# Performance work log

Measured on AMD Instinct MI355X. Metric: run time of the kernel, lower is better.

The kernel has to match this reference:

```python
import jax, jax.numpy as jnp
import numpy as np
import itertools

DIM_X, DIM_Y = 3, 3
MAX_DIGIT = DIM_X * DIM_Y          # 9
NUM_NODES = MAX_DIGIT ** 2         # 81
EMBED = 16
HID = 96
BATCH = 256
ITERS = 4


def determine_edges(dim_x, dim_y):
    md = dim_x * dim_y
    rows = []
    for r in range(md):
        for c in range(md):
            s = {(r, i) for i in range(md)} | {(i, c) for i in range(md)}
            xm, ym = r // dim_x * dim_x, c // dim_y * dim_y
            s |= set(itertools.product(range(xm, xm + dim_x), range(ym, ym + dim_y)))
            s -= {(r, c)}
            rows.append(sorted(i * md + j for i, j in s))
    return np.asarray(rows, dtype=np.int32)  # [81, 20]


def mlp3(x, w0, b0, w1, b1, w2, b2):
    # MLP([a,b,c,d]): two ReLU hidden layers, linear output
    x = jax.nn.relu(x @ w0.T + b0)
    x = jax.nn.relu(x @ w1.T + b1)
    return x @ w2.T + b2


def setup_inputs() -> dict:
    key = jax.random.key(0)
    keys = iter(jax.random.split(key, 40))

    def lin(din, dout):
        kw, kb = jax.random.split(next(keys))
        lim = 1.0 / np.sqrt(din)
        w = jax.random.uniform(kw, (dout, din), jnp.float32, -lim, lim)
        b = jax.random.uniform(kb, (dout,), jnp.float32, -lim, lim)
        return w, b

    embed = jax.random.normal(next(keys), (MAX_DIGIT + 1, EMBED), jnp.float32)

    in_w0, in_b0 = lin(EMBED, HID); in_w1, in_b1 = lin(HID, HID); in_w2, in_b2 = lin(HID, HID)
    f_w0, f_b0 = lin(2 * HID, HID); f_w1, f_b1 = lin(HID, HID); f_w2, f_b2 = lin(HID, HID)
    g_w0, g_b0 = lin(2 * HID, HID); g_w1, g_b1 = lin(HID, HID); g_w2, g_b2 = lin(HID, HID)
    r_w0, r_b0 = lin(HID, HID); r_w1, r_b1 = lin(HID, HID); r_w2, r_b2 = lin(HID, MAX_DIGIT)

    lim = 1.0 / np.sqrt(HID)
    lstm_wih = jax.random.uniform(next(keys), (4 * HID, HID), jnp.float32, -lim, lim)
    lstm_whh = jax.random.uniform(next(keys), (4 * HID, HID), jnp.float32, -lim, lim)
    lstm_bih = jax.random.uniform(next(keys), (4 * HID,), jnp.float32, -lim, lim)
    lstm_bhh = jax.random.uniform(next(keys), (4 * HID,), jnp.float32, -lim, lim)

    grids = jax.random.randint(next(keys), (BATCH, NUM_NODES), 0, MAX_DIGIT + 1)
    c0 = jax.random.normal(next(keys), (BATCH * NUM_NODES, HID), jnp.float32)
    edges = jnp.asarray(determine_edges(DIM_X, DIM_Y))

    return dict(embed=embed,
                in_w0=in_w0, in_b0=in_b0, in_w1=in_w1, in_b1=in_b1, in_w2=in_w2, in_b2=in_b2,
                f_w0=f_w0, f_b0=f_b0, f_w1=f_w1, f_b1=f_b1, f_w2=f_w2, f_b2=f_b2,
                g_w0=g_w0, g_b0=g_b0, g_w1=g_w1, g_b1=g_b1, g_w2=g_w2, g_b2=g_b2,
                lstm_wih=lstm_wih, lstm_whh=lstm_whh, lstm_bih=lstm_bih, lstm_bhh=lstm_bhh,
                r_w0=r_w0, r_b0=r_b0, r_w1=r_w1, r_b1=r_b1, r_w2=r_w2, r_b2=r_b2,
                c0=c0, grids=grids, edges=edges, iters=ITERS)


def reference(embed,
              in_w0, in_b0, in_w1, in_b1, in_w2, in_b2,
              f_w0, f_b0, f_w1, f_b1, f_w2, f_b2,
              g_w0, g_b0, g_w1, g_b1, g_w2, g_b2,
              lstm_wih, lstm_whh, lstm_bih, lstm_bhh,
              r_w0, r_b0, r_w1, r_b1, r_w2, r_b2,
              c0, grids, edges, iters):
    B, N = grids.shape
    K = edges.shape[1]
    emb = embed[grids]                                   # [B, N, EMBED]
    X = mlp3(emb, in_w0, in_b0, in_w1, in_b1, in_w2, in_b2)  # [B, N, HID]
    H = X
    h = X.reshape(B * N, HID)
    c = c0
    outputs = []
    for _ in range(iters):
        # gather neighbor states: [B, N, K, HID]
        Hn = H[:, edges]
        Hs = jnp.broadcast_to(H[:, :, None, :], Hn.shape)
        pair = jnp.concatenate([Hs, Hn], axis=-1)        # [B, N, K, 2*HID]
        M = mlp3(pair, f_w0, f_b0, f_w1, f_b1, f_w2, f_b2).sum(axis=2)  # [B, N, HID]
        gin = mlp3(jnp.concatenate([X, M], axis=-1),
                   g_w0, g_b0, g_w1, g_b1, g_w2, g_b2).reshape(B * N, HID)
        # single-step LSTM (torch gate order: i, f, g, o)
        gates = gin @ lstm_wih.T + lstm_bih + h @ lstm_whh.T + lstm_bhh
        gi, gf, gg, go = jnp.split(gates, 4, axis=-1)
        c = jax.nn.sigmoid(gf) * c + jax.nn.sigmoid(gi) * jnp.tanh(gg)
        h = jax.nn.sigmoid(go) * jnp.tanh(c)
        H = h.reshape(B, N, HID)
        outputs.append(mlp3(H, r_w0, r_b0, r_w1, r_b1, r_w2, r_b2))  # [B, N, MAX_DIGIT]
    return jnp.stack(outputs)  # [iters, B, N, MAX_DIGIT]
```

## Files before the change

### kernel.cpp

```cpp
#include <hip/hip_runtime.h>
#include <hip/hip_bf16.h>

typedef __hip_bfloat16 bf16;
typedef __attribute__((ext_vector_type(8))) short short8;
typedef __attribute__((ext_vector_type(8))) __bf16 bf16x8;
typedef __attribute__((ext_vector_type(4))) float f32x4;

#define BN 20736
#define NNODE 81
#define KNB 20

__device__ inline float bf2f(short s) {
  union { unsigned u; float f; } x; x.u = ((unsigned)(unsigned short)s) << 16; return x.f;
}
__device__ inline short f2bf(float f) {
  __hip_bfloat16 h = __float2bfloat16(f);
  return *reinterpret_cast<short*>(&h);
}

__device__ inline void load_w96(const bf16* __restrict__ W, int ldw, int lr, int lq,
                                bf16x8 wf[6][3]) {
  #pragma unroll
  for (int nt = 0; nt < 6; ++nt)
    #pragma unroll
    for (int ks = 0; ks < 3; ++ks)
      wf[nt][ks] = __builtin_bit_cast(bf16x8,
          *(const short8*)&W[(size_t)(nt * 16 + lr) * ldw + ks * 32 + lq * 8]);
}
__device__ inline void zacc6(f32x4 acc[6]) {
  #pragma unroll
  for (int nt = 0; nt < 6; ++nt) acc[nt] = (f32x4){0.f, 0.f, 0.f, 0.f};
}
__device__ inline void gemm96(const bf16x8 af[3], const bf16x8 wf[6][3], f32x4 acc[6]) {
  #pragma unroll
  for (int ks = 0; ks < 3; ++ks)
    #pragma unroll
    for (int nt = 0; nt < 6; ++nt)
      acc[nt] = __builtin_amdgcn_mfma_f32_16x16x32_bf16(af[ks], wf[nt][ks], acc[nt], 0, 0, 0);
}
__device__ inline void acc_to_xbuf(float* xw, const f32x4 acc[6], int lr, int lq) {
  #pragma unroll
  for (int nt = 0; nt < 6; ++nt)
    #pragma unroll
    for (int r = 0; r < 4; ++r)
      xw[(lq * 4 + r) * 100 + nt * 16 + lr] = acc[nt][r];
}
__device__ inline void xbuf_frag(const float* xw, int lr, int lq,
                                 const float* __restrict__ bias, float bscale,
                                 const bf16* __restrict__ residRow, int act,
                                 bf16x8 af[3]) {
  #pragma unroll
  for (int ks = 0; ks < 3; ++ks) {
    const int c0 = ks * 32 + lq * 8;
    float4 x0 = *(const float4*)&xw[lr * 100 + c0];
    float4 x1 = *(const float4*)&xw[lr * 100 + c0 + 4];
    float xv[8] = {x0.x, x0.y, x0.z, x0.w, x1.x, x1.y, x1.z, x1.w};
    if (bias) {
      float4 b0 = *(const float4*)&bias[c0];
      float4 b1 = *(const float4*)&bias[c0 + 4];
      float bv[8] = {b0.x, b0.y, b0.z, b0.w, b1.x, b1.y, b1.z, b1.w};
      #pragma unroll
      for (int j = 0; j < 8; ++j) xv[j] += bscale * bv[j];
    }
    if (residRow) {
      short8 r8 = *(const short8*)&residRow[c0];
      #pragma unroll
      for (int j = 0; j < 8; ++j) xv[j] += bf2f(r8[j]);
    }
    short8 o;
    #pragma unroll
    for (int j = 0; j < 8; ++j) {
      float v = xv[j];
      if (act) v = fmaxf(v, 0.f);
      o[j] = f2bf(v);
    }
    af[ks] = __builtin_bit_cast(bf16x8, o);
  }
}
__device__ inline void store_frag(bf16* dst, int lq, const bf16x8 af[3]) {
  #pragma unroll
  for (int ks = 0; ks < 3; ++ks)
    *(short8*)&dst[ks * 32 + lq * 8] = __builtin_bit_cast(short8, af[ks]);
}

__global__ __launch_bounds__(256) void prep_k(
    const float* in_w1, const float* in_w2, const float* f_w1, const float* f_w2,
    const float* g_w1, const float* g_w2, const float* r_w0, const float* r_w1,
    const float* r_w2, const float* wih, const float* whh, const float* g_w0,
    const float* f_w0, const float* in_w0, const float* f_b0,
    bf16* inw1b, bf16* inw2b, bf16* fw1b, bf16* fw2b,
    bf16* gw1b, bf16* gw2b, bf16* rw0b, bf16* rw1b,
    bf16* rw2b, bf16* wihb, bf16* whhb, bf16* gw0b,
    bf16* wfnb, bf16* w0pb, float* bias_fn)
{
  int idx = blockIdx.x * 256 + threadIdx.x;
  int y = blockIdx.y;
  const float* src = nullptr; bf16* dst = nullptr; int cnt = 0;
  switch (y) {
    case 0:  src = in_w1; dst = inw1b; cnt = 9216;  break;
    case 1:  src = in_w2; dst = inw2b; cnt = 9216;  break;
    case 2:  src = f_w1;  dst = fw1b;  cnt = 9216;  break;
    case 3:  src = f_w2;  dst = fw2b;  cnt = 9216;  break;
    case 4:  src = g_w1;  dst = gw1b;  cnt = 9216;  break;
    case 5:  src = g_w2;  dst = gw2b;  cnt = 9216;  break;
    case 6:  src = r_w0;  dst = rw0b;  cnt = 9216;  break;
    case 7:  src = r_w1;  dst = rw1b;  cnt = 9216;  break;
    case 8:  src = r_w2;  dst = rw2b;  cnt = 864;   break;
    case 9:  src = wih;   dst = wihb;  cnt = 36864; break;
    case 10: src = whh;   dst = whhb;  cnt = 36864; break;
    case 11: src = g_w0;  dst = gw0b;  cnt = 18432; break;
    case 12: {
      if (idx < 18432) {
        int n = idx / 96, k = idx - n * 96;
        float v = (n < 96) ? f_w0[n * 192 + k] : f_w0[(n - 96) * 192 + 96 + k];
        wfnb[idx] = __float2bfloat16(v);
      }
      return;
    }
    case 13: {
      if (idx < 3072) {
        int n = idx >> 5, k = idx & 31;
        w0pb[idx] = __float2bfloat16(k < 16 ? in_w0[n * 16 + k] : 0.f);
      }
      return;
    }
    default: {
      if (idx < 192) bias_fn[idx] = (idx < 96) ? f_b0[idx] : 0.f;
      return;
    }
  }
  if (idx < cnt) dst[idx] = __float2bfloat16(src[idx]);
}

__global__ __launch_bounds__(256) void embed_k(const float* __restrict__ embed,
                                               const int* __restrict__ grids,
                                               bf16* __restrict__ emb) {
  int idx = blockIdx.x * 256 + threadIdx.x;
  if (idx >= BN * 32) return;
  int r = idx >> 5, k = idx & 31;
  emb[idx] = __float2bfloat16(k < 16 ? embed[grids[r] * 16 + k] : 0.f);
}

__global__ __launch_bounds__(256) void fused_in_k(
    const bf16* __restrict__ emb, const bf16* __restrict__ w0pb, const float* __restrict__ in_b0,
    const bf16* __restrict__ inw1b, const float* __restrict__ in_b1,
    const bf16* __restrict__ inw2b, const float* __restrict__ in_b2,
    const bf16* __restrict__ gw0b, const float* __restrict__ g_b0,
    const bf16* __restrict__ wfnb, const float* __restrict__ bias_fn,
    bf16* __restrict__ X, bf16* __restrict__ Xg, bf16* __restrict__ P)
{
  __shared__ float xbuf[4 * 1600];
  const int t = threadIdx.x, w = t >> 6, lane = t & 63, lr = lane & 15, lq = lane >> 4;
  const int m0 = blockIdx.x * 64 + w * 16;
  float* xw = xbuf + w * 1600;
  bf16x8 wf[6][3]; f32x4 acc[6]; bf16x8 af[3];

  bf16x8 a0 = __builtin_bit_cast(bf16x8, *(const short8*)&emb[(size_t)(m0 + lr) * 32 + lq * 8]);
  #pragma unroll
  for (int nt = 0; nt < 6; ++nt)
    wf[nt][0] = __builtin_bit_cast(bf16x8, *(const short8*)&w0pb[(size_t)(nt * 16 + lr) * 32 + lq * 8]);
  zacc6(acc);
  #pragma unroll
  for (int nt = 0; nt < 6; ++nt)
    acc[nt] = __builtin_amdgcn_mfma_f32_16x16x32_bf16(a0, wf[nt][0], acc[nt], 0, 0, 0);
  acc_to_xbuf(xw, acc, lr, lq); xbuf_frag(xw, lr, lq, in_b0, 1.f, nullptr, 1, af);
  load_w96(inw1b, 96, lr, lq, wf); zacc6(acc); gemm96(af, wf, acc);
  acc_to_xbuf(xw, acc, lr, lq); xbuf_frag(xw, lr, lq, in_b1, 1.f, nullptr, 1, af);
  load_w96(inw2b, 96, lr, lq, wf); zacc6(acc); gemm96(af, wf, acc);
  acc_to_xbuf(xw, acc, lr, lq);
  bf16x8 xf[3];
  xbuf_frag(xw, lr, lq, in_b2, 1.f, nullptr, 0, xf);
  store_frag(&X[(size_t)(m0 + lr) * 96], lq, xf);
  load_w96(gw0b, 192, lr, lq, wf); zacc6(acc); gemm96(xf, wf, acc);
  acc_to_xbuf(xw, acc, lr, lq); xbuf_frag(xw, lr, lq, g_b0, 1.f, nullptr, 0, af);
  store_frag(&Xg[(size_t)(m0 + lr) * 96], lq, af);
  #pragma unroll
  for (int ph = 0; ph < 2; ++ph) {
    load_w96(wfnb + (size_t)ph * 96 * 96, 96, lr, lq, wf); zacc6(acc); gemm96(xf, wf, acc);
    acc_to_xbuf(xw, acc, lr, lq); xbuf_frag(xw, lr, lq, bias_fn + ph * 96, 1.f, nullptr, 0, af);
    store_frag(&P[(size_t)(m0 + lr) * 192 + ph * 96], lq, af);
  }
}

__global__ __launch_bounds__(256) void edge_k(
    const bf16* __restrict__ P, const bf16* __restrict__ w1bf,
    const float* __restrict__ b1, const int* __restrict__ edges,
    bf16* __restrict__ S)
{
  __shared__ short zs[160 * 104];
  const int t = threadIdx.x;
  const int ng0 = blockIdx.x * 2;
  for (int cc = t; cc < 160 * 12; cc += 256) {
    int zrow = cc / 12, c8 = cc - zrow * 12;
    int g = zrow >= 80 ? 1 : 0;
    int row = zrow - g * 80;
    int p = row / 20, j = row - p * 20;
    int gr = (ng0 + g) * 4 + p;
    int b = gr / NNODE, i = gr - b * NNODE;
    int e = edges[i * KNB + j];
    short8 a8 = *(const short8*)&P[(size_t)gr * 192 + c8 * 8];
    short8 n8 = *(const short8*)&P[((size_t)b * NNODE + e) * 192 + 96 + c8 * 8];
    short8 z;
    #pragma unroll
    for (int q = 0; q < 8; ++q)
      z[q] = f2bf(fmaxf(bf2f(a8[q]) + bf2f(n8[q]), 0.f));
    *(short8*)&zs[zrow * 104 + c8 * 8] = z;
  }
  __syncthreads();

  const int w = t >> 6, lane = t & 63, lr = lane & 15, lq = lane >> 4;
  const int g = w >> 1, ch = w & 1, n0 = ch * 48, zb = g * 80;
  const int row0 = (ng0 + g) * 4;

  bf16x8 wf[3][3];
  #pragma unroll
  for (int nt = 0; nt < 3; ++nt)
    #pragma unroll
    for (int ks = 0; ks < 3; ++ks)
      wf[nt][ks] = __builtin_bit_cast(bf16x8,
          *(const short8*)&w1bf[(size_t)(n0 + nt * 16 + lr) * 96 + ks * 32 + lq * 8]);

  f32x4 acc[5][3];
  #pragma unroll
  for (int mt = 0; mt < 5; ++mt)
    #pragma unroll
    for (int nt = 0; nt < 3; ++nt) acc[mt][nt] = (f32x4){0.f, 0.f, 0.f, 0.f};

  #pragma unroll
  for (int ks = 0; ks < 3; ++ks) {
    const int koff = ks * 32 + lq * 8;
    #pragma unroll
    for (int mt = 0; mt < 5; ++mt) {
      bf16x8 af = __builtin_bit_cast(bf16x8, *(const short8*)&zs[(zb + mt * 16 + lr) * 104 + koff]);
      #pragma unroll
      for (int nt = 0; nt < 3; ++nt)
        acc[mt][nt] = __builtin_amdgcn_mfma_f32_16x16x32_bf16(af, wf[nt][ks], acc[mt][nt], 0, 0, 0);
    }
  }

  float bv[3];
  #pragma unroll
  for (int nt = 0; nt < 3; ++nt) bv[nt] = b1[n0 + nt * 16 + lr];
  float nodeacc[4][3];
  #pragma unroll
  for (int pp = 0; pp < 4; ++pp)
    #pragma unroll
    for (int nt = 0; nt < 3; ++nt) nodeacc[pp][nt] = 0.f;
  #pragma unroll
  for (int mt = 0; mt < 5; ++mt)
    #pragma unroll
    for (int nt = 0; nt < 3; ++nt)
      #pragma unroll
      for (int r = 0; r < 4; ++r) {
        int row = mt * 16 + lq * 4 + r;
        int p = row / 20;
        float v = fmaxf(acc[mt][nt][r] + bv[nt], 0.f);
        #pragma unroll
        for (int pp = 0; pp < 4; ++pp)
          nodeacc[pp][nt] += (p == pp) ? v : 0.f;
      }
  #pragma unroll
  for (int pp = 0; pp < 4; ++pp)
    #pragma unroll
    for (int nt = 0; nt < 3; ++nt) {
      float v = nodeacc[pp][nt];
      v += __shfl_xor(v, 16, 64);
      v += __shfl_xor(v, 32, 64);
      if (lq == 0)
        S[(size_t)(row0 + pp) * 96 + n0 + nt * 16 + lr] = __float2bfloat16(v);
    }
}

__global__ __launch_bounds__(256) void fused_mlp_k(
    const bf16* __restrict__ S, const bf16* __restrict__ fw2b, const float* __restrict__ f_b2,
    const bf16* __restrict__ gw0b, const bf16* __restrict__ Xg,
    const bf16* __restrict__ gw1b, const float* __restrict__ g_b1,
    const bf16* __restrict__ gw2b, const float* __restrict__ g_b2,
    bf16* __restrict__ gin)
{
  __shared__ float xbuf[4 * 1600];
  const int t = threadIdx.x, w = t >> 6, lane = t & 63, lr = lane & 15, lq = lane >> 4;
  const int m0 = blockIdx.x * 64 + w * 16;
  float* xw = xbuf + w * 1600;
  bf16x8 wf[6][3]; f32x4 acc[6]; bf16x8 af[3];

  #pragma unroll
  for (int ks = 0; ks < 3; ++ks)
    af[ks] = __builtin_bit_cast(bf16x8, *(const short8*)&S[(size_t)(m0 + lr) * 96 + ks * 32 + lq * 8]);
  load_w96(fw2b, 96, lr, lq, wf); zacc6(acc); gemm96(af, wf, acc);
  acc_to_xbuf(xw, acc, lr, lq); xbuf_frag(xw, lr, lq, f_b2, (float)KNB, nullptr, 0, af);
  load_w96(gw0b + 96, 192, lr, lq, wf); zacc6(acc); gemm96(af, wf, acc);
  acc_to_xbuf(xw, acc, lr, lq);
  xbuf_frag(xw, lr, lq, nullptr, 0.f, &Xg[(size_t)(m0 + lr) * 96], 1, af);
  load_w96(gw1b, 96, lr, lq, wf); zacc6(acc); gemm96(af, wf, acc);
  acc_to_xbuf(xw, acc, lr, lq); xbuf_frag(xw, lr, lq, g_b1, 1.f, nullptr, 1, af);
  load_w96(gw2b, 96, lr, lq, wf); zacc6(acc); gemm96(af, wf, acc);
  acc_to_xbuf(xw, acc, lr, lq); xbuf_frag(xw, lr, lq, g_b2, 1.f, nullptr, 0, af);
  store_frag(&gin[(size_t)(m0 + lr) * 96], lq, af);
}

__global__ __launch_bounds__(256) void lstm_k(
    const bf16* __restrict__ gin, const bf16* __restrict__ Hin,
    const bf16* __restrict__ wihb, const bf16* __restrict__ whhb,
    const float* __restrict__ bih, const float* __restrict__ bhh,
    float* __restrict__ c, bf16* __restrict__ Hout)
{
  const int gslot = blockIdx.x * 4 + (threadIdx.x >> 6);
  const int rt = gslot / 6, knt = gslot - rt * 6;
  const int lane = threadIdx.x & 63, lr = lane & 15, lq = lane >> 4;
  const int m0 = rt * 16, kcol = knt * 16 + lr;

  f32x4 acc[4];
  #pragma unroll
  for (int g = 0; g < 4; ++g) acc[g] = (f32x4){0.f, 0.f, 0.f, 0.f};
  #pragma unroll
  for (int ks = 0; ks < 3; ++ks) {
    const int koff = ks * 32 + lq * 8;
    bf16x8 gf_ = __builtin_bit_cast(bf16x8, *(const short8*)&gin[(size_t)(m0 + lr) * 96 + koff]);
    bf16x8 hf_ = __builtin_bit_cast(bf16x8, *(const short8*)&Hin[(size_t)(m0 + lr) * 96 + koff]);
    #pragma unroll
    for (int g = 0; g < 4; ++g) {
      bf16x8 wi = __builtin_bit_cast(bf16x8, *(const short8*)&wihb[(size_t)(g * 96 + kcol) * 96 + koff]);
      acc[g] = __builtin_amdgcn_mfma_f32_16x16x32_bf16(gf_, wi, acc[g], 0, 0, 0);
      bf16x8 wh = __builtin_bit_cast(bf16x8, *(const short8*)&whhb[(size_t)(g * 96 + kcol) * 96 + koff]);
      acc[g] = __builtin_amdgcn_mfma_f32_16x16x32_bf16(hf_, wh, acc[g], 0, 0, 0);
    }
  }
  float bv[4];
  #pragma unroll
  for (int g = 0; g < 4; ++g) bv[g] = bih[g * 96 + kcol] + bhh[g * 96 + kcol];
  #pragma unroll
  for (int r = 0; r < 4; ++r) {
    int m = m0 + lq * 4 + r;
    size_t idx = (size_t)m * 96 + kcol;
    float gi = acc[0][r] + bv[0];
    float gf = acc[1][r] + bv[1];
    float gg = acc[2][r] + bv[2];
    float go = acc[3][r] + bv[3];
    float si = 1.f / (1.f + expf(-gi));
    float sf = 1.f / (1.f + expf(-gf));
    float so = 1.f / (1.f + expf(-go));
    float tg = tanhf(gg);
    float cn = sf * c[idx] + si * tg;
    c[idx] = cn;
    Hout[idx] = __float2bfloat16(so * tanhf(cn));
  }
}

__global__ __launch_bounds__(256) void fused_out_k(
    const bf16* __restrict__ H,
    const bf16* __restrict__ wfnb, const float* __restrict__ bias_fn, bf16* __restrict__ P,
    const bf16* __restrict__ rw0b, const float* __restrict__ r_b0,
    const bf16* __restrict__ rw1b, const float* __restrict__ r_b1,
    const bf16* __restrict__ rw2b, const float* __restrict__ r_b2,
    float* __restrict__ outp)
{
  __shared__ float xbuf[4 * 1600];
  const int t = threadIdx.x, w = t >> 6, lane = t & 63, lr = lane & 15, lq = lane >> 4;
  const int m0 = blockIdx.x * 64 + w * 16;
  float* xw = xbuf + w * 1600;
  bf16x8 wf[6][3]; f32x4 acc[6]; bf16x8 af[3];

  bf16x8 hf[3];
  #pragma unroll
  for (int ks = 0; ks < 3; ++ks)
    hf[ks] = __builtin_bit_cast(bf16x8, *(const short8*)&H[(size_t)(m0 + lr) * 96 + ks * 32 + lq * 8]);

  #pragma unroll
  for (int ph = 0; ph < 2; ++ph) {
    load_w96(wfnb + (size_t)ph * 96 * 96, 96, lr, lq, wf); zacc6(acc); gemm96(hf, wf, acc);
    acc_to_xbuf(xw, acc, lr, lq); xbuf_frag(xw, lr, lq, bias_fn + ph * 96, 1.f, nullptr, 0, af);
    store_frag(&P[(size_t)(m0 + lr) * 192 + ph * 96], lq, af);
  }
  load_w96(rw0b, 96, lr, lq, wf); zacc6(acc); gemm96(hf, wf, acc);
  acc_to_xbuf(xw, acc, lr, lq); xbuf_frag(xw, lr, lq, r_b0, 1.f, nullptr, 1, af);
  load_w96(rw1b, 96, lr, lq, wf); zacc6(acc); gemm96(af, wf, acc);
  acc_to_xbuf(xw, acc, lr, lq); xbuf_frag(xw, lr, lq, r_b1, 1.f, nullptr, 1, af);
  bf16x8 w9[3];
  #pragma unroll
  for (int ks = 0; ks < 3; ++ks) {
    short8 s = {0, 0, 0, 0, 0, 0, 0, 0};
    if (lr < 9) s = *(const short8*)&rw2b[(size_t)lr * 96 + ks * 32 + lq * 8];
    w9[ks] = __builtin_bit_cast(bf16x8, s);
  }
  f32x4 a9 = (f32x4){0.f, 0.f, 0.f, 0.f};
  #pragma unroll
  for (int ks = 0; ks < 3; ++ks)
    a9 = __builtin_amdgcn_mfma_f32_16x16x32_bf16(af[ks], w9[ks], a9, 0, 0, 0);
  if (lr < 9) {
    float bb = r_b2[lr];
    #pragma unroll
    for (int r = 0; r < 4; ++r)
      outp[(size_t)(m0 + lq * 4 + r) * 9 + lr] = a9[r] + bb;
  }
}

extern "C" void kernel_launch(void* const* d_in, const int* in_sizes, int n_in,
                              void* d_out, int out_size, void* d_ws, size_t ws_size,
                              hipStream_t stream) {
  const float* embed   = (const float*)d_in[0];
  const float* in_w0   = (const float*)d_in[1];
  const float* in_b0   = (const float*)d_in[2];
  const float* in_w1   = (const float*)d_in[3];
  const float* in_b1   = (const float*)d_in[4];
  const float* in_w2   = (const float*)d_in[5];
  const float* in_b2   = (const float*)d_in[6];
  const float* f_w0    = (const float*)d_in[7];
  const float* f_b0    = (const float*)d_in[8];
  const float* f_w1    = (const float*)d_in[9];
  const float* f_b1    = (const float*)d_in[10];
  const float* f_w2    = (const float*)d_in[11];
  const float* f_b2    = (const float*)d_in[12];
  const float* g_w0    = (const float*)d_in[13];
  const float* g_b0    = (const float*)d_in[14];
  const float* g_w1    = (const float*)d_in[15];
  const float* g_b1    = (const float*)d_in[16];
  const float* g_w2    = (const float*)d_in[17];
  const float* g_b2    = (const float*)d_in[18];
  const float* wih     = (const float*)d_in[19];
  const float* whh     = (const float*)d_in[20];
  const float* bih     = (const float*)d_in[21];
  const float* bhh     = (const float*)d_in[22];
  const float* r_w0    = (const float*)d_in[23];
  const float* r_b0    = (const float*)d_in[24];
  const float* r_w1    = (const float*)d_in[25];
  const float* r_b1    = (const float*)d_in[26];
  const float* r_w2    = (const float*)d_in[27];
  const float* r_b2    = (const float*)d_in[28];
  const float* c0      = (const float*)d_in[29];
  const int*   grids   = (const int*)d_in[30];
  const int*   edges   = (const int*)d_in[31];

  float* out = (float*)d_out;
  const int iters = out_size / (BN * 9);

  float* c    = (float*)d_ws;
  bf16* H0    = (bf16*)(c + (size_t)BN * 96);
  bf16* H1    = H0 + (size_t)BN * 96;
  bf16* Xg    = H1 + (size_t)BN * 96;
  bf16* P     = Xg + (size_t)BN * 96;
  bf16* S     = P  + (size_t)BN * 192;
  bf16* gin   = S  + (size_t)BN * 96;
  bf16* emb   = gin + (size_t)BN * 96;
  bf16* w0pb  = emb + (size_t)BN * 32;
  bf16* wfnb  = w0pb + 3072;
  bf16* inw1b = wfnb + 18432;
  bf16* inw2b = inw1b + 9216;
  bf16* fw1b  = inw2b + 9216;
  bf16* fw2b  = fw1b + 9216;
  bf16* gw0b  = fw2b + 9216;
  bf16* gw1b  = gw0b + 18432;
  bf16* gw2b  = gw1b + 9216;
  bf16* rw0b  = gw2b + 9216;
  bf16* rw1b  = rw0b + 9216;
  bf16* rw2b  = rw1b + 9216;
  bf16* wihb  = rw2b + 864;
  bf16* whhb  = wihb + 36864;
  float* bias_fn = (float*)(whhb + 36864);

  prep_k<<<dim3(144, 15), 256, 0, stream>>>(
      in_w1, in_w2, f_w1, f_w2, g_w1, g_w2, r_w0, r_w1, r_w2, wih, whh, g_w0,
      f_w0, in_w0, f_b0,
      inw1b, inw2b, fw1b, fw2b, gw1b, gw2b, rw0b, rw1b, rw2b, wihb, whhb, gw0b,
      wfnb, w0pb, bias_fn);
  embed_k<<<(BN * 32) / 256, 256, 0, stream>>>(embed, grids, emb);
  fused_in_k<<<BN / 64, 256, 0, stream>>>(emb, w0pb, in_b0, inw1b, in_b1, inw2b, in_b2,
                                          gw0b, g_b0, wfnb, bias_fn, H0, Xg, P);
  hipMemcpyAsync(c, c0, (size_t)BN * 96 * sizeof(float), hipMemcpyDeviceToDevice, stream);

  for (int it = 0; it < iters; ++it) {
    bf16* Hin  = (it & 1) ? H1 : H0;
    bf16* Hout = (it & 1) ? H0 : H1;
    edge_k<<<BN / 8, 256, 0, stream>>>(P, fw1b, f_b1, edges, S);
    fused_mlp_k<<<BN / 64, 256, 0, stream>>>(S, fw2b, f_b2, gw0b, Xg, gw1b, g_b1,
                                             gw2b, g_b2, gin);
    lstm_k<<<BN * 6 / 64, 256, 0, stream>>>(gin, Hin, wihb, whhb, bih, bhh, c, Hout);
    fused_out_k<<<BN / 64, 256, 0, stream>>>(Hout, wfnb, bias_fn, P, rw0b, r_b0,
                                             rw1b, r_b1, rw2b, r_b2,
                                             out + (size_t)it * BN * 9);
  }
}
```

Baseline: 370.7 us.

## Split MLP chain N-dimension across wave pairs and fuse f_w2 into edge kernel

The fused MLP kernels now have two waves share each 16-row tile, each computing 48 of the 96 output columns, with block-level barriers to exchange activations through shared memory. Each block therefore covers 32 rows instead of 64, which doubles the grid and halves the weight registers held per wave. Separately, the second edge-MLP GEMM (f_w2 applied to the summed messages, plus the bias times KNB) moves into edge_k via a small padded shared-memory tile. This removes one GEMM and the S round trip from fused_mlp_k, at the cost of extra __syncthreads, duplicated A-operand work across wave pairs, and only two waves active in the edge tail.

```diff
diff --git a/kernel.cpp b/kernel.cpp
--- a/kernel.cpp
+++ b/kernel.cpp
@@ -18,32 +18,32 @@
   return *reinterpret_cast<short*>(&h);
 }
 
-__device__ inline void load_w96(const bf16* __restrict__ W, int ldw, int lr, int lq,
-                                bf16x8 wf[6][3]) {
-  #pragma unroll
-  for (int nt = 0; nt < 6; ++nt)
+__device__ inline void zacc3(f32x4 acc[3]) {
+  #pragma unroll
+  for (int nt = 0; nt < 3; ++nt) acc[nt] = (f32x4){0.f, 0.f, 0.f, 0.f};
+}
+__device__ inline void load_w48(const bf16* __restrict__ W, int ldw, int n0, int lr, int lq,
+                                bf16x8 wf[3][3]) {
+  #pragma unroll
+  for (int nt = 0; nt < 3; ++nt)
     #pragma unroll
     for (int ks = 0; ks < 3; ++ks)
       wf[nt][ks] = __builtin_bit_cast(bf16x8,
-          *(const short8*)&W[(size_t)(nt * 16 + lr) * ldw + ks * 32 + lq * 8]);
-}
-__device__ inline void zacc6(f32x4 acc[6]) {
-  #pragma unroll
-  for (int nt = 0; nt < 6; ++nt) acc[nt] = (f32x4){0.f, 0.f, 0.f, 0.f};
-}
-__device__ inline void gemm96(const bf16x8 af[3], const bf16x8 wf[6][3], f32x4 acc[6]) {
+          *(const short8*)&W[(size_t)(n0 + nt * 16 + lr) * ldw + ks * 32 + lq * 8]);
+}
+__device__ inline void gemm48(const bf16x8 af[3], const bf16x8 wf[3][3], f32x4 acc[3]) {
   #pragma unroll
   for (int ks = 0; ks < 3; ++ks)
     #pragma unroll
-    for (int nt = 0; nt < 6; ++nt)
+    for (int nt = 0; nt < 3; ++nt)
       acc[nt] = __builtin_amdgcn_mfma_f32_16x16x32_bf16(af[ks], wf[nt][ks], acc[nt], 0, 0, 0);
 }
-__device__ inline void acc_to_xbuf(float* xw, const f32x4 acc[6], int lr, int lq) {
-  #pragma unroll
-  for (int nt = 0; nt < 6; ++nt)
+__device__ inline void acc_store_cs(float* xw, const f32x4 acc[3], int lr, int lq, int n0) {
+  #pragma unroll
+  for (int nt = 0; nt < 3; ++nt)
     #pragma unroll
     for (int r = 0; r < 4; ++r)
-      xw[(lq * 4 + r) * 100 + nt * 16 + lr] = acc[nt][r];
+      xw[(lq * 4 + r) * 100 + n0 + nt * 16 + lr] = acc[nt][r];
 }
 __device__ inline void xbuf_frag(const float* xw, int lr, int lq,
                                  const float* __restrict__ bias, float bscale,
@@ -149,47 +149,63 @@
     const bf16* __restrict__ wfnb, const float* __restrict__ bias_fn,
     bf16* __restrict__ X, bf16* __restrict__ Xg, bf16* __restrict__ P)
 {
-  __shared__ float xbuf[4 * 1600];
+  __shared__ float xbuf[2][2][1600];
   const int t = threadIdx.x, w = t >> 6, lane = t & 63, lr = lane & 15, lq = lane >> 4;
-  const int m0 = blockIdx.x * 64 + w * 16;
-  float* xw = xbuf + w * 1600;
-  bf16x8 wf[6][3]; f32x4 acc[6]; bf16x8 af[3];
+  const int mh = w >> 1, ch = w & 1, n0 = ch * 48;
+  const int m0 = blockIdx.x * 32 + mh * 16;
+  float* x0 = xbuf[0][mh];
+  float* x1 = xbuf[1][mh];
+  bf16x8 wf[3][3]; f32x4 acc[3]; bf16x8 af[3];
 
   bf16x8 a0 = __builtin_bit_cast(bf16x8, *(const short8*)&emb[(size_t)(m0 + lr) * 32 + lq * 8]);
   #pragma unroll
-  for (int nt = 0; nt < 6; ++nt)
-    wf[nt][0] = __builtin_bit_cast(bf16x8, *(const short8*)&w0pb[(size_t)(nt * 16 + lr) * 32 + lq * 8]);
-  zacc6(acc);
-  #pragma unroll
-  for (int nt = 0; nt < 6; ++nt)
+  for (int nt = 0; nt < 3; ++nt)
+    wf[nt][0] = __builtin_bit_cast(bf16x8,
+        *(const short8*)&w0pb[(size_t)(n0 + nt * 16 + lr) * 32 + lq * 8]);
+  zacc3(acc);
+  #pragma unroll
+  for (int nt = 0; nt < 3; ++nt)
     acc[nt] = __builtin_amdgcn_mfma_f32_16x16x32_bf16(a0, wf[nt][0], acc[nt], 0, 0, 0);
-  acc_to_xbuf(xw, acc, lr, lq); xbuf_frag(xw, lr, lq, in_b0, 1.f, nullptr, 1, af);
-  load_w96(inw1b, 96, lr, lq, wf); zacc6(acc); gemm96(af, wf, acc);
-  acc_to_xbuf(xw, acc, lr, lq); xbuf_frag(xw, lr, lq, in_b1, 1.f, nullptr, 1, af);
-  load_w96(inw2b, 96, lr, lq, wf); zacc6(acc); gemm96(af, wf, acc);
-  acc_to_xbuf(xw, acc, lr, lq);
+  acc_store_cs(x0, acc, lr, lq, n0);
+  __syncthreads();
+  xbuf_frag(x0, lr, lq, in_b0, 1.f, nullptr, 1, af);
+  load_w48(inw1b, 96, n0, lr, lq, wf); zacc3(acc); gemm48(af, wf, acc);
+  acc_store_cs(x1, acc, lr, lq, n0);
+  __syncthreads();
+  xbuf_frag(x1, lr, lq, in_b1, 1.f, nullptr, 1, af);
+  load_w48(inw2b, 96, n0, lr, lq, wf); zacc3(acc); gemm48(af, wf, acc);
+  acc_store_cs(x0, acc, lr, lq, n0);
+  __syncthreads();
   bf16x8 xf[3];
-  xbuf_frag(xw, lr, lq, in_b2, 1.f, nullptr, 0, xf);
-  store_frag(&X[(size_t)(m0 + lr) * 96], lq, xf);
-  load_w96(gw0b, 192, lr, lq, wf); zacc6(acc); gemm96(xf, wf, acc);
-  acc_to_xbuf(xw, acc, lr, lq); xbuf_frag(xw, lr, lq, g_b0, 1.f, nullptr, 0, af);
-  store_frag(&Xg[(size_t)(m0 + lr) * 96], lq, af);
+  xbuf_frag(x0, lr, lq, in_b2, 1.f, nullptr, 0, xf);
+  if (ch == 0) store_frag(&X[(size_t)(m0 + lr) * 96], lq, xf);
+  load_w48(gw0b, 192, n0, lr, lq, wf); zacc3(acc); gemm48(xf, wf, acc);
+  acc_store_cs(x1, acc, lr, lq, n0);
+  __syncthreads();
+  xbuf_frag(x1, lr, lq, g_b0, 1.f, nullptr, 0, af);
+  if (ch == 0) store_frag(&Xg[(size_t)(m0 + lr) * 96], lq, af);
   #pragma unroll
   for (int ph = 0; ph < 2; ++ph) {
-    load_w96(wfnb + (size_t)ph * 96 * 96, 96, lr, lq, wf); zacc6(acc); gemm96(xf, wf, acc);
-    acc_to_xbuf(xw, acc, lr, lq); xbuf_frag(xw, lr, lq, bias_fn + ph * 96, 1.f, nullptr, 0, af);
-    store_frag(&P[(size_t)(m0 + lr) * 192 + ph * 96], lq, af);
+    float* xb = ph ? x1 : x0;
+    load_w48(wfnb + (size_t)ph * 96 * 96, 96, n0, lr, lq, wf); zacc3(acc); gemm48(xf, wf, acc);
+    acc_store_cs(xb, acc, lr, lq, n0);
+    __syncthreads();
+    xbuf_frag(xb, lr, lq, bias_fn + ph * 96, 1.f, nullptr, 0, af);
+    if (ch == 0) store_frag(&P[(size_t)(m0 + lr) * 192 + ph * 96], lq, af);
   }
 }
 
 __global__ __launch_bounds__(256) void edge_k(
     const bf16* __restrict__ P, const bf16* __restrict__ w1bf,
     const float* __restrict__ b1, const int* __restrict__ edges,
-    bf16* __restrict__ S)
+    const bf16* __restrict__ fw2b, const float* __restrict__ f_b2,
+    bf16* __restrict__ M)
 {
   __shared__ short zs[160 * 104];
+  __shared__ short sbuf[16 * 104];
   const int t = threadIdx.x;
   const int ng0 = blockIdx.x * 2;
+  for (int i = t; i < 8 * 104; i += 256) sbuf[(8 + i / 104) * 104 + (i % 104)] = 0;
   for (int cc = t; cc < 160 * 12; cc += 256) {
     int zrow = cc / 12, c8 = cc - zrow * 12;
     int g = zrow >= 80 ? 1 : 0;
@@ -210,7 +226,6 @@
 
   const int w = t >> 6, lane = t & 63, lr = lane & 15, lq = lane >> 4;
   const int g = w >> 1, ch = w & 1, n0 = ch * 48, zb = g * 80;
-  const int row0 = (ng0 + g) * 4;
 
   bf16x8 wf[3][3];
   #pragma unroll
@@ -267,36 +282,73 @@
       v += __shfl_xor(v, 16, 64);
       v += __shfl_xor(v, 32, 64);
       if (lq == 0)
-        S[(size_t)(row0 + pp) * 96 + n0 + nt * 16 + lr] = __float2bfloat16(v);
-    }
+        sbuf[(g * 4 + pp) * 104 + n0 + nt * 16 + lr] = f2bf(v);
+    }
+  __syncthreads();
+  if (w < 2) {
+    const int mn0 = w * 48;
+    bf16x8 mwf[3][3];
+    #pragma unroll
+    for (int nt = 0; nt < 3; ++nt)
+      #pragma unroll
+      for (int ks = 0; ks < 3; ++ks)
+        mwf[nt][ks] = __builtin_bit_cast(bf16x8,
+            *(const short8*)&fw2b[(size_t)(mn0 + nt * 16 + lr) * 96 + ks * 32 + lq * 8]);
+    f32x4 macc[3];
+    zacc3(macc);
+    #pragma unroll
+    for (int ks = 0; ks < 3; ++ks) {
+      bf16x8 af = __builtin_bit_cast(bf16x8, *(const short8*)&sbuf[lr * 104 + ks * 32 + lq * 8]);
+      #pragma unroll
+      for (int nt = 0; nt < 3; ++nt)
+        macc[nt] = __builtin_amdgcn_mfma_f32_16x16x32_bf16(af, mwf[nt][ks], macc[nt], 0, 0, 0);
+    }
+    #pragma unroll
+    for (int nt = 0; nt < 3; ++nt) {
+      int col = mn0 + nt * 16 + lr;
+      float bb = (float)KNB * f_b2[col];
+      #pragma unroll
+      for (int r = 0; r < 4; ++r) {
+        int row = lq * 4 + r;
+        if (row < 8)
+          M[(size_t)(ng0 * 4 + row) * 96 + col] = __float2bfloat16(macc[nt][r] + bb);
+      }
+    }
+  }
 }
 
 __global__ __launch_bounds__(256) void fused_mlp_k(
-    const bf16* __restrict__ S, const bf16* __restrict__ fw2b, const float* __restrict__ f_b2,
+    const bf16* __restrict__ Min,
     const bf16* __restrict__ gw0b, const bf16* __restrict__ Xg,
     const bf16* __restrict__ gw1b, const float* __restrict__ g_b1,
     const bf16* __restrict__ gw2b, const float* __restrict__ g_b2,
     bf16* __restrict__ gin)
 {
-  __shared__ float xbuf[4 * 1600];
+  __shared__ float xbuf[2][2][1600];
   const int t = threadIdx.x, w = t >> 6, lane = t & 63, lr = lane & 15, lq = lane >> 4;
-  const int m0 = blockIdx.x * 64 + w * 16;
-  float* xw = xbuf + w * 1600;
-  bf16x8 wf[6][3]; f32x4 acc[6]; bf16x8 af[3];
+  const int mh = w >> 1, ch = w & 1, n0 = ch * 48;
+  const int m0 = blockIdx.x * 32 + mh * 16;
+  float* x0 = xbuf[0][mh];
+  float* x1 = xbuf[1][mh];
+  bf16x8 wf[3][3]; f32x4 acc[3]; bf16x8 af[3];
 
   #pragma unroll
   for (int ks = 0; ks < 3; ++ks)
-    af[ks] = __builtin_bit_cast(bf16x8, *(const short8*)&S[(size_t)(m0 + lr) * 96 + ks * 32 + lq * 8]);
-  load_w96(fw2b, 96, lr, lq, wf); zacc6(acc); gemm96(af, wf, acc);
-  acc_to_xbuf(xw, acc, lr, lq); xbuf_frag(xw, lr, lq, f_b2, (float)KNB, nullptr, 0, af);
-  load_w96(gw0b + 96, 192, lr, lq, wf); zacc6(acc); gemm96(af, wf, acc);
-  acc_to_xbuf(xw, acc, lr, lq);
-  xbuf_frag(xw, lr, lq, nullptr, 0.f, &Xg[(size_t)(m0 + lr) * 96], 1, af);
-  load_w96(gw1b, 96, lr, lq, wf); zacc6(acc); gemm96(af, wf, acc);
-  acc_to_xbuf(xw, acc, lr, lq); xbuf_frag(xw, lr, lq, g_b1, 1.f, nullptr, 1, af);
-  load_w96(gw2b, 96, lr, lq, wf); zacc6(acc); gemm96(af, wf, acc);
-  acc_to_xbuf(xw, acc, lr, lq); xbuf_frag(xw, lr, lq, g_b2, 1.f, nullptr, 0, af);
-  store_frag(&gin[(size_t)(m0 + lr) * 96], lq, af);
+    af[ks] = __builtin_bit_cast(bf16x8,
+        *(const short8*)&Min[(size_t)(m0 + lr) * 96 + ks * 32 + lq * 8]);
+  load_w48(gw0b + 96, 192, n0, lr, lq, wf); zacc3(acc); gemm48(af, wf, acc);
+  acc_store_cs(x0, acc, lr, lq, n0);
+  __syncthreads();
+  xbuf_frag(x0, lr, lq, nullptr, 0.f, &Xg[(size_t)(m0 + lr) * 96], 1, af);
+  load_w48(gw1b, 96, n0, lr, lq, wf); zacc3(acc); gemm48(af, wf, acc);
+  acc_store_cs(x1, acc, lr, lq, n0);
+  __syncthreads();
+  xbuf_frag(x1, lr, lq, g_b1, 1.f, nullptr, 1, af);
+  load_w48(gw2b, 96, n0, lr, lq, wf); zacc3(acc); gemm48(af, wf, acc);
+  acc_store_cs(x0, acc, lr, lq, n0);
+  __syncthreads();
+  xbuf_frag(x0, lr, lq, g_b2, 1.f, nullptr, 0, af);
+  if (ch == 0) store_frag(&gin[(size_t)(m0 + lr) * 96], lq, af);
 }
 
 __global__ __launch_bounds__(256) void lstm_k(
@@ -355,43 +407,55 @@
     const bf16* __restrict__ rw2b, const float* __restrict__ r_b2,
     float* __restrict__ outp)
 {
-  __shared__ float xbuf[4 * 1600];
+  __shared__ float xbuf[2][2][1600];
   const int t = threadIdx.x, w = t >> 6, lane = t & 63, lr = lane & 15, lq = lane >> 4;
-  const int m0 = blockIdx.x * 64 + w * 16;
-  float* xw = xbuf + w * 1600;
-  bf16x8 wf[6][3]; f32x4 acc[6]; bf16x8 af[3];
+  const int mh = w >> 1, ch = w & 1, n0 = ch * 48;
+  const int m0 = blockIdx.x * 32 + mh * 16;
+  float* x0 = xbuf[0][mh];
+  float* x1 = xbuf[1][mh];
+  bf16x8 wf[3][3]; f32x4 acc[3]; bf16x8 af[3];
 
   bf16x8 hf[3];
   #pragma unroll
   for (int ks = 0; ks < 3; ++ks)
-    hf[ks] = __builtin_bit_cast(bf16x8, *(const short8*)&H[(size_t)(m0 + lr) * 96 + ks * 32 + lq * 8]);
+    hf[ks] = __builtin_bit_cast(bf16x8,
+        *(const short8*)&H[(size_t)(m0 + lr) * 96 + ks * 32 + lq * 8]);
 
   #pragma unroll
   for (int ph = 0; ph < 2; ++ph) {
-    load_w96(wfnb + (size_t)ph * 96 * 96, 96, lr, lq, wf); zacc6(acc); gemm96(hf, wf, acc);
-    acc_to_xbuf(xw, acc, lr, lq); xbuf_frag(xw, lr, lq, bias_fn + ph * 96, 1.f, nullptr, 0, af);
-    store_frag(&P[(size_t)(m0 + lr) * 192 + ph * 96], lq, af);
-  }
-  load_w96(rw0b, 96, lr, lq, wf); zacc6(acc); gemm96(hf, wf, acc);
-  acc_to_xbuf(xw, acc, lr, lq); xbuf_frag(xw, lr, lq, r_b0, 1.f, nullptr, 1, af);
-  load_w96(rw1b, 96, lr, lq, wf); zacc6(acc); gemm96(af, wf, acc);
-  acc_to_xbuf(xw, acc, lr, lq); xbuf_frag(xw, lr, lq, r_b1, 1.f, nullptr, 1, af);
-  bf16x8 w9[3];
-  #pragma unroll
-  for (int ks = 0; ks < 3; ++ks) {
-    short8 s = {0, 0, 0, 0, 0, 0, 0, 0};
-    if (lr < 9) s = *(const short8*)&rw2b[(size_t)lr * 96 + ks * 32 + lq * 8];
-    w9[ks] = __builtin_bit_cast(bf16x8, s);
-  }
-  f32x4 a9 = (f32x4){0.f, 0.f, 0.f, 0.f};
-  #pragma unroll
-  for (int ks = 0; ks < 3; ++ks)
-    a9 = __builtin_amdgcn_mfma_f32_16x16x32_bf16(af[ks], w9[ks], a9, 0, 0, 0);
-  if (lr < 9) {
-    float bb = r_b2[lr];
-    #pragma unroll
-    for (int r = 0; r < 4; ++r)
-      outp[(size_t)(m0 + lq * 4 + r) * 9 + lr] = a9[r] + bb;
+    float* xb = ph ? x1 : x0;
+    load_w48(wfnb + (size_t)ph * 96 * 96, 96, n0, lr, lq, wf); zacc3(acc); gemm48(hf, wf, acc);
+    acc_store_cs(xb, acc, lr, lq, n0);
+    __syncthreads();
+    xbuf_frag(xb, lr, lq, bias_fn + ph * 96, 1.f, nullptr, 0, af);
+    if (ch == 0) store_frag(&P[(size_t)(m0 + lr) * 192 + ph * 96], lq, af);
+  }
+  load_w48(rw0b, 96, n0, lr, lq, wf); zacc3(acc); gemm48(hf, wf, acc);
+  acc_store_cs(x0, acc, lr, lq, n0);
+  __syncthreads();
+  xbuf_frag(x0, lr, lq, r_b0, 1.f, nullptr, 1, af);
+  load_w48(rw1b, 96, n0, lr, lq, wf); zacc3(acc); gemm48(af, wf, acc);
+  acc_store_cs(x1, acc, lr, lq, n0);
+  __syncthreads();
+  xbuf_frag(x1, lr, lq, r_b1, 1.f, nullptr, 1, af);
+  if (ch == 0) {
+    bf16x8 w9[3];
+    #pragma unroll
+    for (int ks = 0; ks < 3; ++ks) {
+      short8 s = {0, 0, 0, 0, 0, 0, 0, 0};
+      if (lr < 9) s = *(const short8*)&rw2b[(size_t)lr * 96 + ks * 32 + lq * 8];
+      w9[ks] = __builtin_bit_cast(bf16x8, s);
+    }
+    f32x4 a9 = (f32x4){0.f, 0.f, 0.f, 0.f};
+    #pragma unroll
+    for (int ks = 0; ks < 3; ++ks)
+      a9 = __builtin_amdgcn_mfma_f32_16x16x32_bf16(af[ks], w9[ks], a9, 0, 0, 0);
+    if (lr < 9) {
+      float bb = r_b2[lr];
+      #pragma unroll
+      for (int r = 0; r < 4; ++r)
+        outp[(size_t)(m0 + lq * 4 + r) * 9 + lr] = a9[r] + bb;
+    }
   }
 }
 
@@ -439,8 +503,8 @@
   bf16* H1    = H0 + (size_t)BN * 96;
   bf16* Xg    = H1 + (size_t)BN * 96;
   bf16* P     = Xg + (size_t)BN * 96;
-  bf16* S     = P  + (size_t)BN * 192;
-  bf16* gin   = S  + (size_t)BN * 96;
+  bf16* Mb    = P  + (size_t)BN * 192;
+  bf16* gin   = Mb + (size_t)BN * 96;
   bf16* emb   = gin + (size_t)BN * 96;
   bf16* w0pb  = emb + (size_t)BN * 32;
   bf16* wfnb  = w0pb + 3072;
@@ -464,18 +528,17 @@
       inw1b, inw2b, fw1b, fw2b, gw1b, gw2b, rw0b, rw1b, rw2b, wihb, whhb, gw0b,
       wfnb, w0pb, bias_fn);
   embed_k<<<(BN * 32) / 256, 256, 0, stream>>>(embed, grids, emb);
-  fused_in_k<<<BN / 64, 256, 0, stream>>>(emb, w0pb, in_b0, inw1b, in_b1, inw2b, in_b2,
+  fused_in_k<<<BN / 32, 256, 0, stream>>>(emb, w0pb, in_b0, inw1b, in_b1, inw2b, in_b2,
                                           gw0b, g_b0, wfnb, bias_fn, H0, Xg, P);
   hipMemcpyAsync(c, c0, (size_t)BN * 96 * sizeof(float), hipMemcpyDeviceToDevice, stream);
 
   for (int it = 0; it < iters; ++it) {
     bf16* Hin  = (it & 1) ? H1 : H0;
     bf16* Hout = (it & 1) ? H0 : H1;
-    edge_k<<<BN / 8, 256, 0, stream>>>(P, fw1b, f_b1, edges, S);
-    fused_mlp_k<<<BN / 64, 256, 0, stream>>>(S, fw2b, f_b2, gw0b, Xg, gw1b, g_b1,
-                                             gw2b, g_b2, gin);
+    edge_k<<<BN / 8, 256, 0, stream>>>(P, fw1b, f_b1, edges, fw2b, f_b2, Mb);
+    fused_mlp_k<<<BN / 32, 256, 0, stream>>>(Mb, gw0b, Xg, gw1b, g_b1, gw2b, g_b2, gin);
     lstm_k<<<BN * 6 / 64, 256, 0, stream>>>(gin, Hin, wihb, whhb, bih, bhh, c, Hout);
-    fused_out_k<<<BN / 64, 256, 0, stream>>>(Hout, wfnb, bias_fn, P, rw0b, r_b0,
+    fused_out_k<<<BN / 32, 256, 0, stream>>>(Hout, wfnb, bias_fn, P, rw0b, r_b0,
                                              rw1b, r_b1, rw2b, r_b2,
                                              out + (size_t)it * BN * 9);
   }
```

New measurement: 361.4 us. -2.5%, faster.
